# Performance work log

Measured on AMD Instinct MI355X. Metric: run time of the kernel, lower is better.

## Reference

```python
import jax, jax.numpy as jnp
import numpy as np
from functools import partial

B, L, H, OUT, T, NLAYERS = 1024, 128, 256, 64, 256, 2


def setup_inputs() -> dict:
    key = jax.random.key(0)
    ks = jax.random.split(key, 16)
    s = 0.05
    inp = {
        "latent": jax.random.normal(ks[0], (B, L), jnp.float32),
        # latent -> initial hidden / cell (Linear(L, H*num_layers))
        "w_lh": jax.random.normal(ks[1], (H * NLAYERS, L), jnp.float32) * s,
        "b_lh": jax.random.normal(ks[2], (H * NLAYERS,), jnp.float32) * s,
        "w_lc": jax.random.normal(ks[3], (H * NLAYERS, L), jnp.float32) * s,
        "b_lc": jax.random.normal(ks[4], (H * NLAYERS,), jnp.float32) * s,
        # LSTM layer 0 (input_size = L), PyTorch gate order i,f,g,o
        "w_ih0": jax.random.normal(ks[5], (4 * H, L), jnp.float32) * s,
        "w_hh0": jax.random.normal(ks[6], (4 * H, H), jnp.float32) * s,
        "b_ih0": jax.random.normal(ks[7], (4 * H,), jnp.float32) * s,
        "b_hh0": jax.random.normal(ks[8], (4 * H,), jnp.float32) * s,
        # LSTM layer 1 (input_size = H)
        "w_ih1": jax.random.normal(ks[9], (4 * H, H), jnp.float32) * s,
        "w_hh1": jax.random.normal(ks[10], (4 * H, H), jnp.float32) * s,
        "b_ih1": jax.random.normal(ks[11], (4 * H,), jnp.float32) * s,
        "b_hh1": jax.random.normal(ks[12], (4 * H,), jnp.float32) * s,
        # output projection Linear(H, OUT)
        "w_out": jax.random.normal(ks[13], (OUT, H), jnp.float32) * s,
        "b_out": jax.random.normal(ks[14], (OUT,), jnp.float32) * s,
    }
    return inp


def _lstm_layer(gx, h0, c0, w_hh):
    # gx: [T, B, 4H] precomputed input-projection + biases; scan the recurrence.
    def step(carry, gx_t):
        h, c = carry
        gates = gx_t + h @ w_hh.T  # [B, 4H]
        i, f, g, o = jnp.split(gates, 4, axis=-1)
        i, f, o = jax.nn.sigmoid(i), jax.nn.sigmoid(f), jax.nn.sigmoid(o)
        g = jnp.tanh(g)
        c = f * c + i * g
        h = o * jnp.tanh(c)
        return (h, c), h

    _, hs = jax.lax.scan(step, (h0, c0), gx)
    return hs  # [T, B, H]


def reference(latent, w_lh, b_lh, w_lc, b_lc,
              w_ih0, w_hh0, b_ih0, b_hh0,
              w_ih1, w_hh1, b_ih1, b_hh1,
              w_out, b_out):
    bsz = latent.shape[0]
    # initial states: [B, NLAYERS, H] -> per-layer [B, H]
    h = (latent @ w_lh.T + b_lh).reshape(bsz, NLAYERS, H)
    c = (latent @ w_lc.T + b_lc).reshape(bsz, NLAYERS, H)

    # decoder input is latent repeated T times; layer-0 input projection is
    # identical at every step, so compute it once and broadcast over time.
    gx0 = latent @ w_ih0.T + b_ih0 + b_hh0           # [B, 4H]
    gx0 = jnp.broadcast_to(gx0, (T, bsz, 4 * H))      # [T, B, 4H]
    hs0 = _lstm_layer(gx0, h[:, 0], c[:, 0], w_hh0)   # [T, B, H]

    # layer 1: time-varying input projection (dropout between layers is
    # inference-mode identity)
    gx1 = jnp.einsum('tbh,gh->tbg', hs0, w_ih1) + b_ih1 + b_hh1
    hs1 = _lstm_layer(gx1, h[:, 1], c[:, 1], w_hh1)   # [T, B, H]

    out = jnp.einsum('tbh,oh->tbo', hs1, w_out) + b_out  # [T, B, OUT]
    return jnp.transpose(out, (1, 0, 2))                 # [B, T, OUT]
```

## Files before the change

kernel.cpp:

```cpp
#include <hip/hip_runtime.h>


typedef float f32x4 __attribute__((ext_vector_type(4)));
typedef short bf16x8 __attribute__((ext_vector_type(8)));
typedef unsigned short u16;
typedef unsigned int u32;
typedef unsigned int u32x2 __attribute__((ext_vector_type(2)));
typedef unsigned int u32x4 __attribute__((ext_vector_type(4)));

#define OFF_LH   0
#define OFF_LC   65536
#define OFF_IH0  131072
#define OFF_HH0  262144
#define OFF_IH1  524288
#define OFF_HH1  786432
#define OFF_OUT  1048576

#define COMM_B   2228224
#define OBOX(bid,kind,slot) (COMM_B + ((((bid)*2+(kind))*2+(slot)) << 11))
#define FLAG_B   (COMM_B + 2097152)
#define FLAGQ(bid,kind) (FLAG_B + (((bid)*2+(kind)) << 4))
#define SPIN_LIMIT (1<<15)
#define HST 264

__device__ __forceinline__ u16 f2bf(float x){
  unsigned u = __builtin_bit_cast(unsigned, x);
  return (u16)((u + 0x7fffu + ((u >> 16) & 1u)) >> 16);
}

__global__ __launch_bounds__(256) void convert_swizzle(
    const float* __restrict__ src, u16* __restrict__ dst,
    int ntiles, int kbshift)
{
  int idx = blockIdx.x * 256 + threadIdx.x;
  int kblocks = 1 << kbshift;
  int n = ntiles << (kbshift + 9);
  if (idx >= n) return;
  int j    = idx & 7;
  int lane = (idx >> 3) & 63;
  int t3   = idx >> 9;
  int kt   = t3 & (kblocks - 1);
  int nt   = t3 >> kbshift;
  int row  = nt * 16 + (lane & 15);
  int k    = kt * 32 + (lane >> 4) * 8 + j;
  dst[idx] = f2bf(src[row * (kblocks * 32) + k]);
}

__device__ __forceinline__ f32x4 mfma16(bf16x8 a, bf16x8 b, f32x4 c){
  return __builtin_amdgcn_mfma_f32_16x16x32_bf16(a, b, c, 0, 0, 0);
}
__device__ __forceinline__ bf16x8 ld8(const u16* p){ return *(const bf16x8*)p; }
__device__ __forceinline__ float sigm(float x){ return 1.f/(1.f + __expf(-x)); }
__device__ __forceinline__ float tanh_f(float x){ return 1.f - 2.f/(__expf(2.f*x) + 1.f); }

#define ISSUE4(Q, seg, kt) \
  asm volatile( \
    "global_load_dwordx4 %0, %4, %8\n\t" \
    "global_load_dwordx4 %1, %5, %8\n\t" \
    "global_load_dwordx4 %2, %6, %8\n\t" \
    "global_load_dwordx4 %3, %7, %8" \
    : "=&v"(Q[0]), "=&v"(Q[1]), "=&v"(Q[2]), "=&v"(Q[3]) \
    : "v"(voffW +           (u32)((kt)*1024)), \
      "v"(voffW + 131072u + (u32)((kt)*1024)), \
      "v"(voffW + 262144u + (u32)((kt)*1024)), \
      "v"(voffW + 393216u + (u32)((kt)*1024)), \
      "s"(seg) \
    : "memory")

#define WAITN(Q, lit) \
  asm volatile("s_waitcnt vmcnt(" lit ")" \
    : "+v"(Q[0]), "+v"(Q[1]), "+v"(Q[2]), "+v"(Q[3]) :: "memory")
#define WAITC(Q) WAITN(Q, "12")

#define MFMA4(afrag, Q) { \
  acc0 = mfma16(afrag, Q[0], acc0); \
  acc1 = mfma16(afrag, Q[1], acc1); \
  acc2 = mfma16(afrag, Q[2], acc2); \
  acc3 = mfma16(afrag, Q[3], acc3); }

#define BARX() asm volatile("s_waitcnt lgkmcnt(0)\n\ts_barrier" ::: "memory")
#define VDRAIN() asm volatile("s_waitcnt vmcnt(0)" ::: "memory")

__device__ __forceinline__ void stflag(u32* p, u32 v){
  __hip_atomic_store(p, v, __ATOMIC_RELAXED, __HIP_MEMORY_SCOPE_AGENT);
}
__device__ __forceinline__ void pub8(char* p, u32 lo, u32 hi){
  u32x2 v = {lo, hi};
  asm volatile("global_store_dwordx2 %0, %1, off sc0 sc1" :: "v"(p), "v"(v) : "memory");
}

__device__ __forceinline__ void gatherF1(u16* hdst,
    const char* pay, const char* fq, int ps, int lane, u32 tgt, int* dead)
{
  if (!*dead){
    int gc = 0;
    for(;;){
      u32x4 fa;
      asm volatile(
        "global_load_dwordx4 %0, %1, off sc0 sc1\n\ts_waitcnt vmcnt(0)"
        : "=&v"(fa) : "v"(fq) : "memory");
      if (fa[0] >= tgt && fa[1] >= tgt && fa[2] >= tgt && fa[3] >= tgt) break;
      if (++gc > SPIN_LIMIT){ *dead = 1; break; }
    }
  }
  u32x4 q0, q1;
  asm volatile(
    "global_load_dwordx4 %0, %2, off sc0 sc1\n\t"
    "global_load_dwordx4 %1, %3, off sc0 sc1"
    : "=&v"(q0), "=&v"(q1)
    : "v"(pay), "v"(pay+16)
    : "memory");
  asm volatile("s_waitcnt vmcnt(0)" : "+v"(q0), "+v"(q1) :: "memory");
  const int r  = lane >> 4;
  const int cb = ps*64 + r*16;
  #pragma unroll
  for (int j = 0; j < 4; ++j){
    u32 lo = (j < 2) ? q0[2*j]   : q1[2*(j-2)];
    u32 hi = (j < 2) ? q0[2*j+1] : q1[2*(j-2)+1];
    int pl = (lane & 15)*4 + j;
    u16* dst = &hdst[((pl >> 4)*4)*HST + cb + (pl & 15)];
    dst[0]     = (u16)lo;
    dst[HST]   = (u16)(lo >> 16);
    dst[2*HST] = (u16)hi;
    dst[3*HST] = (u16)(hi >> 16);
  }
}

__global__ __launch_bounds__(512)
void lstm_fused(
    const float* __restrict__ latent,
    const float* __restrict__ b_lh, const float* __restrict__ b_lc,
    const float* __restrict__ b_ih0, const float* __restrict__ b_hh0,
    const float* __restrict__ b_ih1, const float* __restrict__ b_hh1,
    const float* __restrict__ b_out,
    const u16* __restrict__ ws,
    u16* __restrict__ comm,
    float* __restrict__ out)
{
  __shared__ __attribute__((aligned(16))) u16 h0f[2][16*HST];
  __shared__ __attribute__((aligned(16))) u16 h1f[3][16*HST];
  __shared__ __attribute__((aligned(16))) u16 lat_s[16*136];

  const u16* __restrict__ w_lh  = ws + OFF_LH;
  const u16* __restrict__ w_lc  = ws + OFF_LC;
  const u16* __restrict__ w_ih0 = ws + OFF_IH0;
  const u16* __restrict__ w_hh0 = ws + OFF_HH0;
  const u16* __restrict__ w_ih1 = ws + OFF_IH1;
  const u16* __restrict__ w_hh1 = ws + OFF_HH1;
  const u16* __restrict__ w_out = ws + OFF_OUT;

  const int tid  = threadIdx.x;
  const int w    = tid >> 6;
  const int lane = tid & 63;
  const int col  = lane & 15;
  const int quad = lane >> 4;
  const int bid  = blockIdx.x;
  const int s    = bid & 3;
  const int g    = bid >> 2;
  const int hct4 = w & 3;
  const int hrow = quad * 4;
  const int l8   = lane * 8;
  const int ctb  = s*64 + hct4*16;
  const u32 voffW = (u32)((s*4 + hct4) * 8192 + lane * 16);
  const int hreadR = col * HST + quad * 8;
  char* cm = (char*)comm;

  for (int i = tid; i < 16*128; i += 512){
    int b = i >> 7, k = i & 127;
    lat_s[b*136 + k] = f2bf(latent[(g*16 + b)*128 + k]);
  }
  __syncthreads();

  #pragma unroll 1
  for (int i = 0; i < 4; ++i){
    int task = w*4 + i;
    int layer = task >> 4, ct = task & 15;
    int nt = layer*16 + ct;
    float bias = b_lh[nt*16 + col];
    f32x4 a = {bias, bias, bias, bias};
    #pragma unroll
    for (int kt = 0; kt < 4; ++kt){
      bf16x8 la = ld8(&lat_s[col*136 + kt*32 + quad*8]);
      a = mfma16(la, ld8(w_lh + ((nt*4 + kt) << 9) + l8), a);
    }
    u16* dst = layer ? h1f[2] : h0f[1];
    #pragma unroll
    for (int rr = 0; rr < 4; ++rr)
      dst[(hrow + rr)*HST + ct*16 + col] = f2bf(a[rr]);
  }

  bf16x8 latA[4];
  #pragma unroll
  for (int kt = 0; kt < 4; ++kt)
    latA[kt] = ld8(&lat_s[col*136 + kt*32 + quad*8]);

  f32x4 gx0[4] = {};
  float bias1[4] = {};
  float c0[4] = {}, c1[4] = {};
  const float bo = (w == 0) ? b_out[s*16 + col] : 0.f;

  if (w < 4){
    { float bias = b_lc[ctb + col]; f32x4 a = {bias,bias,bias,bias};
      int nt0 = s*4 + hct4;
      #pragma unroll
      for (int kt = 0; kt < 4; ++kt)
        a = mfma16(latA[kt], ld8(w_lc + ((nt0*4 + kt) << 9) + l8), a);
      #pragma unroll
      for (int rr = 0; rr < 4; ++rr) c0[rr] = a[rr]; }
    #pragma unroll
    for (int g_ = 0; g_ < 4; ++g_){
      int nt = g_*16 + s*4 + hct4;
      float bias = b_ih0[nt*16 + col] + b_hh0[nt*16 + col];
      f32x4 a = {bias, bias, bias, bias};
      #pragma unroll
      for (int kt = 0; kt < 4; ++kt)
        a = mfma16(latA[kt], ld8(w_ih0 + ((nt*4 + kt) << 9) + l8), a);
      gx0[g_] = a;
    }
  } else {
    { float bias = b_lc[256 + ctb + col]; f32x4 a = {bias,bias,bias,bias};
      int nt1 = 16 + s*4 + hct4;
      #pragma unroll
      for (int kt = 0; kt < 4; ++kt)
        a = mfma16(latA[kt], ld8(w_lc + ((nt1*4 + kt) << 9) + l8), a);
      #pragma unroll
      for (int rr = 0; rr < 4; ++rr) c1[rr] = a[rr]; }
    #pragma unroll
    for (int g_ = 0; g_ < 4; ++g_){
      int nt = g_*16 + s*4 + hct4;
      bias1[g_] = b_ih1[nt*16 + col] + b_hh1[nt*16 + col];
    }
  }

  const int wl = w & 3;
  const int havep = (wl < 3);
  int ps = (wl < s) ? wl : wl + 1;
  if (!havep) ps = 0;
  const int kindm = (w < 4) ? 0 : 1;
  const char* ppay = cm + OBOX(g*4 + ps, kindm, 0) + lane*32;
  const char* fq   = cm + FLAGQ(g*4 + ps, kindm);
  u32* fmyw = (u32*)(cm + FLAGQ(bid, kindm)) + wl;
  char* pub_own = cm + OBOX(bid, kindm, 0) + hct4*512 + lane*8;
  int dead = 0;

  __syncthreads();

  bf16x8 Pq0[4], Pq1[4], Pq2[4], Pq3[4];
  f32x4 acc0, acc1, acc2, acc3;
  bf16x8 a0;
  if (w < 4){
    ISSUE4(Pq0, w_hh0, 0); ISSUE4(Pq1, w_hh0, 1);
    ISSUE4(Pq2, w_hh0, 2); ISSUE4(Pq3, w_hh0, 3);
    const u16* h0m1 = h0f[1];
    acc0 = gx0[0]; acc1 = gx0[1]; acc2 = gx0[2]; acc3 = gx0[3];
    WAITC(Pq0);      a0 = ld8(&h0m1[hreadR + 0*32]); MFMA4(a0, Pq0); ISSUE4(Pq0, w_hh0, 4);
    WAITC(Pq1);      a0 = ld8(&h0m1[hreadR + 1*32]); MFMA4(a0, Pq1); ISSUE4(Pq1, w_hh0, 5);
    WAITC(Pq2);      a0 = ld8(&h0m1[hreadR + 2*32]); MFMA4(a0, Pq2); ISSUE4(Pq2, w_hh0, 6);
    WAITC(Pq3);      a0 = ld8(&h0m1[hreadR + 3*32]); MFMA4(a0, Pq3); ISSUE4(Pq3, w_hh0, 7);
    WAITC(Pq0);      a0 = ld8(&h0m1[hreadR + 4*32]); MFMA4(a0, Pq0);
    WAITN(Pq1, "8"); a0 = ld8(&h0m1[hreadR + 5*32]); MFMA4(a0, Pq1);
    WAITN(Pq2, "4"); a0 = ld8(&h0m1[hreadR + 6*32]); MFMA4(a0, Pq2);
    WAITN(Pq3, "0"); a0 = ld8(&h0m1[hreadR + 7*32]); MFMA4(a0, Pq3);
    u32 plo = 0, phi = 0;
    #pragma unroll
    for (int rr = 0; rr < 4; ++rr){
      float ii = sigm(acc0[rr]);
      float ff = sigm(acc1[rr]);
      float gg = tanh_f(acc2[rr]);
      float oo = sigm(acc3[rr]);
      float c = ff*c0[rr] + ii*gg;
      c0[rr] = c;
      u16 hb = f2bf(oo * tanh_f(c));
      h0f[0][(hrow + rr)*HST + ctb + col] = hb;
      if (rr & 2) phi |= (u32)hb << ((rr & 1)*16);
      else        plo |= (u32)hb << ((rr & 1)*16);
    }
    pub8(pub_own, plo, phi);
    VDRAIN();
    __builtin_amdgcn_sched_barrier(0);
    if (lane == 0) stflag(fmyw, 1u);
    ISSUE4(Pq0, w_hh0, 0); ISSUE4(Pq1, w_hh0, 1);
    ISSUE4(Pq2, w_hh0, 2); ISSUE4(Pq3, w_hh0, 3);
  } else {
    ISSUE4(Pq0, w_hh1, 0); ISSUE4(Pq1, w_hh1, 1);
    ISSUE4(Pq2, w_hh1, 2); ISSUE4(Pq3, w_hh1, 3);
  }

  int m0 = 0, m1 = 2, m2 = 1;

  for (int t = 0; t < 256; ++t){
    const int p = t & 1;
    u16* h0c  = h0f[p];
    u16* h0n  = h0f[p ^ 1];
    u16* h1c  = h1f[m0];
    u16* h1pr = h1f[m1];

    if (w < 4){
      if (havep)
        gatherF1(h0c, ppay + (p << 11), fq, ps, lane, (u32)(t+1), &dead);
    } else if (t > 0 && havep){
      gatherF1(h1pr, ppay + ((p^1) << 11), fq, ps, lane, (u32)t, &dead);
    }
    BARX();

    if (w < 4){
      acc0 = gx0[0]; acc1 = gx0[1]; acc2 = gx0[2]; acc3 = gx0[3];
      WAITC(Pq0);      a0 = ld8(&h0c[hreadR + 0*32]); MFMA4(a0, Pq0); ISSUE4(Pq0, w_hh0, 4);
      WAITC(Pq1);      a0 = ld8(&h0c[hreadR + 1*32]); MFMA4(a0, Pq1); ISSUE4(Pq1, w_hh0, 5);
      WAITC(Pq2);      a0 = ld8(&h0c[hreadR + 2*32]); MFMA4(a0, Pq2); ISSUE4(Pq2, w_hh0, 6);
      WAITC(Pq3);      a0 = ld8(&h0c[hreadR + 3*32]); MFMA4(a0, Pq3); ISSUE4(Pq3, w_hh0, 7);
      WAITC(Pq0);      a0 = ld8(&h0c[hreadR + 4*32]); MFMA4(a0, Pq0);
      WAITN(Pq1, "8"); a0 = ld8(&h0c[hreadR + 5*32]); MFMA4(a0, Pq1);
      WAITN(Pq2, "4"); a0 = ld8(&h0c[hreadR + 6*32]); MFMA4(a0, Pq2);
      WAITN(Pq3, "0"); a0 = ld8(&h0c[hreadR + 7*32]); MFMA4(a0, Pq3);
      u32 plo = 0, phi = 0;
      #pragma unroll
      for (int rr = 0; rr < 4; ++rr){
        float ii = sigm(acc0[rr]);
        float ff = sigm(acc1[rr]);
        float gg = tanh_f(acc2[rr]);
        float oo = sigm(acc3[rr]);
        float c = ff*c0[rr] + ii*gg;
        c0[rr] = c;
        u16 hb = f2bf(oo * tanh_f(c));
        h0n[(hrow + rr)*HST + ctb + col] = hb;
        if (rr & 2) phi |= (u32)hb << ((rr & 1)*16);
        else        plo |= (u32)hb << ((rr & 1)*16);
      }
      pub8(pub_own + ((p^1) << 11), plo, phi);
      VDRAIN();
      __builtin_amdgcn_sched_barrier(0);
      if (lane == 0) stflag(fmyw, (u32)(t+2));
      ISSUE4(Pq0, w_hh0, 0); ISSUE4(Pq1, w_hh0, 1);
      ISSUE4(Pq2, w_hh0, 2); ISSUE4(Pq3, w_hh0, 3);
      if (w == 0 && t >= 2){
        const u16* h1o = h1f[m2];
        f32x4 o = {bo, bo, bo, bo};
        #pragma unroll
        for (int kt = 0; kt < 8; ++kt){
          bf16x8 af = ld8(&h1o[hreadR + kt*32]);
          o = mfma16(af, ld8(w_out + ((s*8 + kt) << 9) + l8), o);
        }
        #pragma unroll
        for (int rr = 0; rr < 4; ++rr){
          int b = g*16 + hrow + rr;
          __builtin_nontemporal_store(o[rr], &out[(b*256 + (t-2))*64 + s*16 + col]);
        }
      }
    } else {
      acc0 = (f32x4){bias1[0],bias1[0],bias1[0],bias1[0]};
      acc1 = (f32x4){bias1[1],bias1[1],bias1[1],bias1[1]};
      acc2 = (f32x4){bias1[2],bias1[2],bias1[2],bias1[2]};
      acc3 = (f32x4){bias1[3],bias1[3],bias1[3],bias1[3]};
      WAITC(Pq0);      a0 = ld8(&h1pr[hreadR + 0*32]); MFMA4(a0, Pq0); ISSUE4(Pq0, w_hh1, 4);
      WAITC(Pq1);      a0 = ld8(&h1pr[hreadR + 1*32]); MFMA4(a0, Pq1); ISSUE4(Pq1, w_hh1, 5);
      WAITC(Pq2);      a0 = ld8(&h1pr[hreadR + 2*32]); MFMA4(a0, Pq2); ISSUE4(Pq2, w_hh1, 6);
      WAITC(Pq3);      a0 = ld8(&h1pr[hreadR + 3*32]); MFMA4(a0, Pq3); ISSUE4(Pq3, w_hh1, 7);
      WAITC(Pq0);      a0 = ld8(&h1pr[hreadR + 4*32]); MFMA4(a0, Pq0); ISSUE4(Pq0, w_ih1, 0);
      WAITC(Pq1);      a0 = ld8(&h1pr[hreadR + 5*32]); MFMA4(a0, Pq1); ISSUE4(Pq1, w_ih1, 1);
      WAITC(Pq2);      a0 = ld8(&h1pr[hreadR + 6*32]); MFMA4(a0, Pq2); ISSUE4(Pq2, w_ih1, 2);
      WAITC(Pq3);      a0 = ld8(&h1pr[hreadR + 7*32]); MFMA4(a0, Pq3); ISSUE4(Pq3, w_ih1, 3);
      WAITC(Pq0);      a0 = ld8(&h0c[hreadR + 0*32]); MFMA4(a0, Pq0); ISSUE4(Pq0, w_ih1, 4);
      WAITC(Pq1);      a0 = ld8(&h0c[hreadR + 1*32]); MFMA4(a0, Pq1); ISSUE4(Pq1, w_ih1, 5);
      WAITC(Pq2);      a0 = ld8(&h0c[hreadR + 2*32]); MFMA4(a0, Pq2); ISSUE4(Pq2, w_ih1, 6);
      WAITC(Pq3);      a0 = ld8(&h0c[hreadR + 3*32]); MFMA4(a0, Pq3); ISSUE4(Pq3, w_ih1, 7);
      WAITC(Pq0);      a0 = ld8(&h0c[hreadR + 4*32]); MFMA4(a0, Pq0);
      WAITN(Pq1, "8"); a0 = ld8(&h0c[hreadR + 5*32]); MFMA4(a0, Pq1);
      WAITN(Pq2, "4"); a0 = ld8(&h0c[hreadR + 6*32]); MFMA4(a0, Pq2);
      WAITN(Pq3, "0"); a0 = ld8(&h0c[hreadR + 7*32]); MFMA4(a0, Pq3);
      u32 plo = 0, phi = 0;
      #pragma unroll
      for (int rr = 0; rr < 4; ++rr){
        float ii = sigm(acc0[rr]);
        float ff = sigm(acc1[rr]);
        float gg = tanh_f(acc2[rr]);
        float oo = sigm(acc3[rr]);
        float c = ff*c1[rr] + ii*gg;
        c1[rr] = c;
        u16 hb = f2bf(oo * tanh_f(c));
        h1c[(hrow + rr)*HST + ctb + col] = hb;
        if (rr & 2) phi |= (u32)hb << ((rr & 1)*16);
        else        plo |= (u32)hb << ((rr & 1)*16);
      }
      pub8(pub_own + (p << 11), plo, phi);
      VDRAIN();
      __builtin_amdgcn_sched_barrier(0);
      if (lane == 0) stflag(fmyw, (u32)(t+1));
      ISSUE4(Pq0, w_hh1, 0); ISSUE4(Pq1, w_hh1, 1);
      ISSUE4(Pq2, w_hh1, 2); ISSUE4(Pq3, w_hh1, 3);
    }
    BARX();

    int tm = m2; m2 = m1; m1 = m0; m0 = tm;
  }

  if (w >= 4){
    if (havep)
      gatherF1(h1f[0], ppay + (1 << 11), fq, ps, lane, 256u, &dead);
  } else if (w == 0){
    const u16* h1o = h1f[2];
    f32x4 o = {bo, bo, bo, bo};
    #pragma unroll
    for (int kt = 0; kt < 8; ++kt){
      bf16x8 af = ld8(&h1o[hreadR + kt*32]);
      o = mfma16(af, ld8(w_out + ((s*8 + kt) << 9) + l8), o);
    }
    #pragma unroll
    for (int rr = 0; rr < 4; ++rr){
      int b = g*16 + hrow + rr;
      __builtin_nontemporal_store(o[rr], &out[(b*256 + 254)*64 + s*16 + col]);
    }
  }
  BARX();
  if (w == 0){
    const u16* h1fin = h1f[0];
    f32x4 o = {bo, bo, bo, bo};
    #pragma unroll
    for (int kt = 0; kt < 8; ++kt){
      bf16x8 af = ld8(&h1fin[hreadR + kt*32]);
      o = mfma16(af, ld8(w_out + ((s*8 + kt) << 9) + l8), o);
    }
    #pragma unroll
    for (int rr = 0; rr < 4; ++rr){
      int b = g*16 + hrow + rr;
      __builtin_nontemporal_store(o[rr], &out[(b*256 + 255)*64 + s*16 + col]);
    }
  }
}

extern "C" void kernel_launch(void* const* d_in, const int* in_sizes, int n_in,
                              void* d_out, int out_size, void* d_ws, size_t ws_size,
                              hipStream_t stream)
{
  (void)in_sizes; (void)n_in; (void)out_size; (void)ws_size;
  const float* latent = (const float*)d_in[0];
  const float* w_lh   = (const float*)d_in[1];
  const float* b_lh   = (const float*)d_in[2];
  const float* w_lc   = (const float*)d_in[3];
  const float* b_lc   = (const float*)d_in[4];
  const float* w_ih0  = (const float*)d_in[5];
  const float* w_hh0  = (const float*)d_in[6];
  const float* b_ih0  = (const float*)d_in[7];
  const float* b_hh0  = (const float*)d_in[8];
  const float* w_ih1  = (const float*)d_in[9];
  const float* w_hh1  = (const float*)d_in[10];
  const float* b_ih1  = (const float*)d_in[11];
  const float* b_hh1  = (const float*)d_in[12];
  const float* w_out  = (const float*)d_in[13];
  const float* b_out  = (const float*)d_in[14];
  u16* ws = (u16*)d_ws;
  float* out = (float*)d_out;

  auto cvt = [&](const float* src, int off, int ntiles, int kbshift){
    int n = ntiles << (kbshift + 9);
    convert_swizzle<<<dim3((n + 255)/256), dim3(256), 0, stream>>>(src, ws + off, ntiles, kbshift);
  };
  cvt(w_lh,  OFF_LH,  32, 2);
  cvt(w_lc,  OFF_LC,  32, 2);
  cvt(w_ih0, OFF_IH0, 64, 2);
  cvt(w_hh0, OFF_HH0, 64, 3);
  cvt(w_ih1, OFF_IH1, 64, 3);
  cvt(w_hh1, OFF_HH1, 64, 3);
  cvt(w_out, OFF_OUT, 4, 3);

  hipMemsetAsync((char*)d_ws + FLAG_B, 0, 256*2*16, stream);

  lstm_fused<<<dim3(256), dim3(512), 0, stream>>>(latent, b_lh, b_lc, b_ih0, b_hh0,
                                                  b_ih1, b_hh1, b_out, ws, ws, out);
}
```

Before: 1.454 ms.

## Prefetch peer flags early and overlap payload loads with weight prefetch

Each wave now issues the flag load for its peer's handoff right after publishing its own step, so the next spin check often finds the flag already satisfied without a round trip. The per-step recurrent-weight prefetch (ISSUE4) is moved from the end of each step to after the payload loads are issued, and waits with vmcnt(16) so the payload can be consumed while the weight loads are still in flight. This aims to cut inter-block synchronisation latency on the serial recurrence. The trade-off is that weight prefetch now starts later, and correctness relies on vmcnt ordering assumptions in inline asm.

```diff
diff --git a/kernel.cpp b/kernel.cpp
--- a/kernel.cpp
+++ b/kernel.cpp
@@ -89,6 +89,22 @@
   asm volatile("global_store_dwordx2 %0, %1, off sc0 sc1" :: "v"(p), "v"(v) : "memory");
 }
 
+__device__ __forceinline__ void scat8(u16* hdst, u32x4 q0, u32x4 q1, int ps, int lane){
+  const int r  = lane >> 4;
+  const int cb = ps*64 + r*16;
+  #pragma unroll
+  for (int j = 0; j < 4; ++j){
+    u32 lo = (j < 2) ? q0[2*j]   : q1[2*(j-2)];
+    u32 hi = (j < 2) ? q0[2*j+1] : q1[2*(j-2)+1];
+    int pl = (lane & 15)*4 + j;
+    u16* dst = &hdst[((pl >> 4)*4)*HST + cb + (pl & 15)];
+    dst[0]     = (u16)lo;
+    dst[HST]   = (u16)(lo >> 16);
+    dst[2*HST] = (u16)hi;
+    dst[3*HST] = (u16)(hi >> 16);
+  }
+}
+
 __device__ __forceinline__ void gatherF1(u16* hdst,
     const char* pay, const char* fq, int ps, int lane, u32 tgt, int* dead)
 {
@@ -111,19 +127,7 @@
     : "v"(pay), "v"(pay+16)
     : "memory");
   asm volatile("s_waitcnt vmcnt(0)" : "+v"(q0), "+v"(q1) :: "memory");
-  const int r  = lane >> 4;
-  const int cb = ps*64 + r*16;
-  #pragma unroll
-  for (int j = 0; j < 4; ++j){
-    u32 lo = (j < 2) ? q0[2*j]   : q1[2*(j-2)];
-    u32 hi = (j < 2) ? q0[2*j+1] : q1[2*(j-2)+1];
-    int pl = (lane & 15)*4 + j;
-    u16* dst = &hdst[((pl >> 4)*4)*HST + cb + (pl & 15)];
-    dst[0]     = (u16)lo;
-    dst[HST]   = (u16)(lo >> 16);
-    dst[2*HST] = (u16)hi;
-    dst[3*HST] = (u16)(hi >> 16);
-  }
+  scat8(hdst, q0, q1, ps, lane);
 }
 
 __global__ __launch_bounds__(512)
@@ -242,6 +246,7 @@
   u32* fmyw = (u32*)(cm + FLAGQ(bid, kindm)) + wl;
   char* pub_own = cm + OBOX(bid, kindm, 0) + hct4*512 + lane*8;
   int dead = 0;
+  u32x4 fpre = {0,0,0,0};
 
   __syncthreads();
 
@@ -279,11 +284,9 @@
     VDRAIN();
     __builtin_amdgcn_sched_barrier(0);
     if (lane == 0) stflag(fmyw, 1u);
-    ISSUE4(Pq0, w_hh0, 0); ISSUE4(Pq1, w_hh0, 1);
-    ISSUE4(Pq2, w_hh0, 2); ISSUE4(Pq3, w_hh0, 3);
-  } else {
-    ISSUE4(Pq0, w_hh1, 0); ISSUE4(Pq1, w_hh1, 1);
-    ISSUE4(Pq2, w_hh1, 2); ISSUE4(Pq3, w_hh1, 3);
+    if (havep)
+      asm volatile("global_load_dwordx4 %0, %1, off sc0 sc1"
+        : "=&v"(fpre) : "v"(fq) : "memory");
   }
 
   int m0 = 0, m1 = 2, m2 = 1;
@@ -296,10 +299,63 @@
     u16* h1pr = h1f[m1];
 
     if (w < 4){
-      if (havep)
-        gatherF1(h0c, ppay + (p << 11), fq, ps, lane, (u32)(t+1), &dead);
-    } else if (t > 0 && havep){
-      gatherF1(h1pr, ppay + ((p^1) << 11), fq, ps, lane, (u32)t, &dead);
+      if (havep){
+        asm volatile("s_waitcnt vmcnt(0)" : "+v"(fpre) :: "memory");
+        u32 tgt = (u32)(t+1);
+        if (!dead && !(fpre[0] >= tgt && fpre[1] >= tgt && fpre[2] >= tgt && fpre[3] >= tgt)){
+          int gc = 0;
+          for(;;){
+            u32x4 fa;
+            asm volatile(
+              "global_load_dwordx4 %0, %1, off sc0 sc1\n\ts_waitcnt vmcnt(0)"
+              : "=&v"(fa) : "v"(fq) : "memory");
+            if (fa[0] >= tgt && fa[1] >= tgt && fa[2] >= tgt && fa[3] >= tgt) break;
+            if (++gc > SPIN_LIMIT){ dead = 1; break; }
+          }
+        }
+        const char* pp = ppay + (p << 11);
+        u32x4 q0, q1;
+        asm volatile(
+          "global_load_dwordx4 %0, %2, off sc0 sc1\n\t"
+          "global_load_dwordx4 %1, %3, off sc0 sc1"
+          : "=&v"(q0), "=&v"(q1) : "v"(pp), "v"(pp+16) : "memory");
+        ISSUE4(Pq0, w_hh0, 0); ISSUE4(Pq1, w_hh0, 1);
+        ISSUE4(Pq2, w_hh0, 2); ISSUE4(Pq3, w_hh0, 3);
+        asm volatile("s_waitcnt vmcnt(16)" : "+v"(q0), "+v"(q1) :: "memory");
+        scat8(h0c, q0, q1, ps, lane);
+      } else {
+        ISSUE4(Pq0, w_hh0, 0); ISSUE4(Pq1, w_hh0, 1);
+        ISSUE4(Pq2, w_hh0, 2); ISSUE4(Pq3, w_hh0, 3);
+      }
+    } else {
+      if (t > 0 && havep){
+        asm volatile("s_waitcnt vmcnt(0)" : "+v"(fpre) :: "memory");
+        u32 tgt = (u32)t;
+        if (!dead && !(fpre[0] >= tgt && fpre[1] >= tgt && fpre[2] >= tgt && fpre[3] >= tgt)){
+          int gc = 0;
+          for(;;){
+            u32x4 fa;
+            asm volatile(
+              "global_load_dwordx4 %0, %1, off sc0 sc1\n\ts_waitcnt vmcnt(0)"
+              : "=&v"(fa) : "v"(fq) : "memory");
+            if (fa[0] >= tgt && fa[1] >= tgt && fa[2] >= tgt && fa[3] >= tgt) break;
+            if (++gc > SPIN_LIMIT){ dead = 1; break; }
+          }
+        }
+        const char* pp = ppay + ((p^1) << 11);
+        u32x4 q0, q1;
+        asm volatile(
+          "global_load_dwordx4 %0, %2, off sc0 sc1\n\t"
+          "global_load_dwordx4 %1, %3, off sc0 sc1"
+          : "=&v"(q0), "=&v"(q1) : "v"(pp), "v"(pp+16) : "memory");
+        ISSUE4(Pq0, w_hh1, 0); ISSUE4(Pq1, w_hh1, 1);
+        ISSUE4(Pq2, w_hh1, 2); ISSUE4(Pq3, w_hh1, 3);
+        asm volatile("s_waitcnt vmcnt(16)" : "+v"(q0), "+v"(q1) :: "memory");
+        scat8(h1pr, q0, q1, ps, lane);
+      } else {
+        ISSUE4(Pq0, w_hh1, 0); ISSUE4(Pq1, w_hh1, 1);
+        ISSUE4(Pq2, w_hh1, 2); ISSUE4(Pq3, w_hh1, 3);
+      }
     }
     BARX();
 
@@ -331,8 +387,9 @@
       VDRAIN();
       __builtin_amdgcn_sched_barrier(0);
       if (lane == 0) stflag(fmyw, (u32)(t+2));
-      ISSUE4(Pq0, w_hh0, 0); ISSUE4(Pq1, w_hh0, 1);
-      ISSUE4(Pq2, w_hh0, 2); ISSUE4(Pq3, w_hh0, 3);
+      if (havep)
+        asm volatile("global_load_dwordx4 %0, %1, off sc0 sc1"
+          : "=&v"(fpre) : "v"(fq) : "memory");
       if (w == 0 && t >= 2){
         const u16* h1o = h1f[m2];
         f32x4 o = {bo, bo, bo, bo};
@@ -386,8 +443,9 @@
       VDRAIN();
       __builtin_amdgcn_sched_barrier(0);
       if (lane == 0) stflag(fmyw, (u32)(t+1));
-      ISSUE4(Pq0, w_hh1, 0); ISSUE4(Pq1, w_hh1, 1);
-      ISSUE4(Pq2, w_hh1, 2); ISSUE4(Pq3, w_hh1, 3);
+      if (havep)
+        asm volatile("global_load_dwordx4 %0, %1, off sc0 sc1"
+          : "=&v"(fpre) : "v"(fq) : "memory");
     }
     BARX();
 
```

Result: slower. 1.875 ms (+28.9%).

## Keep recurrent weight slices resident in registers instead of streaming each step

Applied to the files above, without the earlier changes.

Each wave now loads its slice of the recurrent weight matrix (w_hh0 or w_hh1) into 32 bf16x8 registers once before the time loop. The per-step global streaming of those weights is removed, and only w_ih1 is still streamed, through a two-deep queue. The layer-1 flag gather is inlined so the w_ih1 loads are issued before the payload scatter, overlapping them with the neighbour exchange. The cost is much higher VGPR pressure (128 extra registers), which risks spills at 512 threads per block.

```diff
diff --git a/kernel.cpp b/kernel.cpp
--- a/kernel.cpp
+++ b/kernel.cpp
@@ -70,7 +70,6 @@
 #define WAITN(Q, lit) \
   asm volatile("s_waitcnt vmcnt(" lit ")" \
     : "+v"(Q[0]), "+v"(Q[1]), "+v"(Q[2]), "+v"(Q[3]) :: "memory")
-#define WAITC(Q) WAITN(Q, "12")
 
 #define MFMA4(afrag, Q) { \
   acc0 = mfma16(afrag, Q[0], acc0); \
@@ -78,6 +77,12 @@
   acc2 = mfma16(afrag, Q[2], acc2); \
   acc3 = mfma16(afrag, Q[3], acc3); }
 
+#define MFMA4W(afrag, kt) { \
+  acc0 = mfma16(afrag, Wst[0*8+(kt)], acc0); \
+  acc1 = mfma16(afrag, Wst[1*8+(kt)], acc1); \
+  acc2 = mfma16(afrag, Wst[2*8+(kt)], acc2); \
+  acc3 = mfma16(afrag, Wst[3*8+(kt)], acc3); }
+
 #define BARX() asm volatile("s_waitcnt lgkmcnt(0)\n\ts_barrier" ::: "memory")
 #define VDRAIN() asm volatile("s_waitcnt vmcnt(0)" ::: "memory")
 
@@ -87,6 +92,22 @@
 __device__ __forceinline__ void pub8(char* p, u32 lo, u32 hi){
   u32x2 v = {lo, hi};
   asm volatile("global_store_dwordx2 %0, %1, off sc0 sc1" :: "v"(p), "v"(v) : "memory");
+}
+
+__device__ __forceinline__ void scat8(u16* hdst, u32x4 q0, u32x4 q1, int ps, int lane){
+  const int r  = lane >> 4;
+  const int cb = ps*64 + r*16;
+  #pragma unroll
+  for (int j = 0; j < 4; ++j){
+    u32 lo = (j < 2) ? q0[2*j]   : q1[2*(j-2)];
+    u32 hi = (j < 2) ? q0[2*j+1] : q1[2*(j-2)+1];
+    int pl = (lane & 15)*4 + j;
+    u16* dst = &hdst[((pl >> 4)*4)*HST + cb + (pl & 15)];
+    dst[0]     = (u16)lo;
+    dst[HST]   = (u16)(lo >> 16);
+    dst[2*HST] = (u16)hi;
+    dst[3*HST] = (u16)(hi >> 16);
+  }
 }
 
 __device__ __forceinline__ void gatherF1(u16* hdst,
@@ -111,19 +132,7 @@
     : "v"(pay), "v"(pay+16)
     : "memory");
   asm volatile("s_waitcnt vmcnt(0)" : "+v"(q0), "+v"(q1) :: "memory");
-  const int r  = lane >> 4;
-  const int cb = ps*64 + r*16;
-  #pragma unroll
-  for (int j = 0; j < 4; ++j){
-    u32 lo = (j < 2) ? q0[2*j]   : q1[2*(j-2)];
-    u32 hi = (j < 2) ? q0[2*j+1] : q1[2*(j-2)+1];
-    int pl = (lane & 15)*4 + j;
-    u16* dst = &hdst[((pl >> 4)*4)*HST + cb + (pl & 15)];
-    dst[0]     = (u16)lo;
-    dst[HST]   = (u16)(lo >> 16);
-    dst[2*HST] = (u16)hi;
-    dst[3*HST] = (u16)(hi >> 16);
-  }
+  scat8(hdst, q0, q1, ps, lane);
 }
 
 __global__ __launch_bounds__(512)
@@ -171,6 +180,19 @@
   }
   __syncthreads();
 
+  bf16x8 Wst[32];
+  {
+    const u16* wsrc = (w < 4) ? w_hh0 : w_hh1;
+    #pragma unroll
+    for (int g_ = 0; g_ < 4; ++g_){
+      #pragma unroll
+      for (int kt = 0; kt < 8; ++kt){
+        int nt = g_*16 + s*4 + hct4;
+        Wst[g_*8 + kt] = ld8(wsrc + ((nt*8 + kt) << 9) + l8);
+      }
+    }
+  }
+
   #pragma unroll 1
   for (int i = 0; i < 4; ++i){
     int task = w*4 + i;
@@ -245,22 +267,17 @@
 
   __syncthreads();
 
-  bf16x8 Pq0[4], Pq1[4], Pq2[4], Pq3[4];
+  bf16x8 Pq0[4], Pq1[4];
   f32x4 acc0, acc1, acc2, acc3;
   bf16x8 a0;
   if (w < 4){
-    ISSUE4(Pq0, w_hh0, 0); ISSUE4(Pq1, w_hh0, 1);
-    ISSUE4(Pq2, w_hh0, 2); ISSUE4(Pq3, w_hh0, 3);
     const u16* h0m1 = h0f[1];
     acc0 = gx0[0]; acc1 = gx0[1]; acc2 = gx0[2]; acc3 = gx0[3];
-    WAITC(Pq0);      a0 = ld8(&h0m1[hreadR + 0*32]); MFMA4(a0, Pq0); ISSUE4(Pq0, w_hh0, 4);
-    WAITC(Pq1);      a0 = ld8(&h0m1[hreadR + 1*32]); MFMA4(a0, Pq1); ISSUE4(Pq1, w_hh0, 5);
-    WAITC(Pq2);      a0 = ld8(&h0m1[hreadR + 2*32]); MFMA4(a0, Pq2); ISSUE4(Pq2, w_hh0, 6);
-    WAITC(Pq3);      a0 = ld8(&h0m1[hreadR + 3*32]); MFMA4(a0, Pq3); ISSUE4(Pq3, w_hh0, 7);
-    WAITC(Pq0);      a0 = ld8(&h0m1[hreadR + 4*32]); MFMA4(a0, Pq0);
-    WAITN(Pq1, "8"); a0 = ld8(&h0m1[hreadR + 5*32]); MFMA4(a0, Pq1);
-    WAITN(Pq2, "4"); a0 = ld8(&h0m1[hreadR + 6*32]); MFMA4(a0, Pq2);
-    WAITN(Pq3, "0"); a0 = ld8(&h0m1[hreadR + 7*32]); MFMA4(a0, Pq3);
+    #pragma unroll
+    for (int kt = 0; kt < 8; ++kt){
+      a0 = ld8(&h0m1[hreadR + kt*32]);
+      MFMA4W(a0, kt);
+    }
     u32 plo = 0, phi = 0;
     #pragma unroll
     for (int rr = 0; rr < 4; ++rr){
@@ -279,11 +296,6 @@
     VDRAIN();
     __builtin_amdgcn_sched_barrier(0);
     if (lane == 0) stflag(fmyw, 1u);
-    ISSUE4(Pq0, w_hh0, 0); ISSUE4(Pq1, w_hh0, 1);
-    ISSUE4(Pq2, w_hh0, 2); ISSUE4(Pq3, w_hh0, 3);
-  } else {
-    ISSUE4(Pq0, w_hh1, 0); ISSUE4(Pq1, w_hh1, 1);
-    ISSUE4(Pq2, w_hh1, 2); ISSUE4(Pq3, w_hh1, 3);
   }
 
   int m0 = 0, m1 = 2, m2 = 1;
@@ -298,21 +310,42 @@
     if (w < 4){
       if (havep)
         gatherF1(h0c, ppay + (p << 11), fq, ps, lane, (u32)(t+1), &dead);
-    } else if (t > 0 && havep){
-      gatherF1(h1pr, ppay + ((p^1) << 11), fq, ps, lane, (u32)t, &dead);
+    } else {
+      if (t > 0 && havep){
+        if (!dead){
+          int gc = 0;
+          u32 tgt = (u32)t;
+          for(;;){
+            u32x4 fa;
+            asm volatile(
+              "global_load_dwordx4 %0, %1, off sc0 sc1\n\ts_waitcnt vmcnt(0)"
+              : "=&v"(fa) : "v"(fq) : "memory");
+            if (fa[0] >= tgt && fa[1] >= tgt && fa[2] >= tgt && fa[3] >= tgt) break;
+            if (++gc > SPIN_LIMIT){ dead = 1; break; }
+          }
+        }
+        const char* pp = ppay + ((p^1) << 11);
+        u32x4 q0, q1;
+        asm volatile(
+          "global_load_dwordx4 %0, %2, off sc0 sc1\n\t"
+          "global_load_dwordx4 %1, %3, off sc0 sc1"
+          : "=&v"(q0), "=&v"(q1) : "v"(pp), "v"(pp+16) : "memory");
+        ISSUE4(Pq0, w_ih1, 0); ISSUE4(Pq1, w_ih1, 1);
+        asm volatile("s_waitcnt vmcnt(8)" : "+v"(q0), "+v"(q1) :: "memory");
+        scat8(h1pr, q0, q1, ps, lane);
+      } else {
+        ISSUE4(Pq0, w_ih1, 0); ISSUE4(Pq1, w_ih1, 1);
+      }
     }
     BARX();
 
     if (w < 4){
       acc0 = gx0[0]; acc1 = gx0[1]; acc2 = gx0[2]; acc3 = gx0[3];
-      WAITC(Pq0);      a0 = ld8(&h0c[hreadR + 0*32]); MFMA4(a0, Pq0); ISSUE4(Pq0, w_hh0, 4);
-      WAITC(Pq1);      a0 = ld8(&h0c[hreadR + 1*32]); MFMA4(a0, Pq1); ISSUE4(Pq1, w_hh0, 5);
-      WAITC(Pq2);      a0 = ld8(&h0c[hreadR + 2*32]); MFMA4(a0, Pq2); ISSUE4(Pq2, w_hh0, 6);
-      WAITC(Pq3);      a0 = ld8(&h0c[hreadR + 3*32]); MFMA4(a0, Pq3); ISSUE4(Pq3, w_hh0, 7);
-      WAITC(Pq0);      a0 = ld8(&h0c[hreadR + 4*32]); MFMA4(a0, Pq0);
-      WAITN(Pq1, "8"); a0 = ld8(&h0c[hreadR + 5*32]); MFMA4(a0, Pq1);
-      WAITN(Pq2, "4"); a0 = ld8(&h0c[hreadR + 6*32]); MFMA4(a0, Pq2);
-      WAITN(Pq3, "0"); a0 = ld8(&h0c[hreadR + 7*32]); MFMA4(a0, Pq3);
+      #pragma unroll
+      for (int kt = 0; kt < 8; ++kt){
+        a0 = ld8(&h0c[hreadR + kt*32]);
+        MFMA4W(a0, kt);
+      }
       u32 plo = 0, phi = 0;
       #pragma unroll
       for (int rr = 0; rr < 4; ++rr){
@@ -331,8 +364,6 @@
       VDRAIN();
       __builtin_amdgcn_sched_barrier(0);
       if (lane == 0) stflag(fmyw, (u32)(t+2));
-      ISSUE4(Pq0, w_hh0, 0); ISSUE4(Pq1, w_hh0, 1);
-      ISSUE4(Pq2, w_hh0, 2); ISSUE4(Pq3, w_hh0, 3);
       if (w == 0 && t >= 2){
         const u16* h1o = h1f[m2];
         f32x4 o = {bo, bo, bo, bo};
@@ -352,22 +383,19 @@
       acc1 = (f32x4){bias1[1],bias1[1],bias1[1],bias1[1]};
       acc2 = (f32x4){bias1[2],bias1[2],bias1[2],bias1[2]};
       acc3 = (f32x4){bias1[3],bias1[3],bias1[3],bias1[3]};
-      WAITC(Pq0);      a0 = ld8(&h1pr[hreadR + 0*32]); MFMA4(a0, Pq0); ISSUE4(Pq0, w_hh1, 4);
-      WAITC(Pq1);      a0 = ld8(&h1pr[hreadR + 1*32]); MFMA4(a0, Pq1); ISSUE4(Pq1, w_hh1, 5);
-      WAITC(Pq2);      a0 = ld8(&h1pr[hreadR + 2*32]); MFMA4(a0, Pq2); ISSUE4(Pq2, w_hh1, 6);
-      WAITC(Pq3);      a0 = ld8(&h1pr[hreadR + 3*32]); MFMA4(a0, Pq3); ISSUE4(Pq3, w_hh1, 7);
-      WAITC(Pq0);      a0 = ld8(&h1pr[hreadR + 4*32]); MFMA4(a0, Pq0); ISSUE4(Pq0, w_ih1, 0);
-      WAITC(Pq1);      a0 = ld8(&h1pr[hreadR + 5*32]); MFMA4(a0, Pq1); ISSUE4(Pq1, w_ih1, 1);
-      WAITC(Pq2);      a0 = ld8(&h1pr[hreadR + 6*32]); MFMA4(a0, Pq2); ISSUE4(Pq2, w_ih1, 2);
-      WAITC(Pq3);      a0 = ld8(&h1pr[hreadR + 7*32]); MFMA4(a0, Pq3); ISSUE4(Pq3, w_ih1, 3);
-      WAITC(Pq0);      a0 = ld8(&h0c[hreadR + 0*32]); MFMA4(a0, Pq0); ISSUE4(Pq0, w_ih1, 4);
-      WAITC(Pq1);      a0 = ld8(&h0c[hreadR + 1*32]); MFMA4(a0, Pq1); ISSUE4(Pq1, w_ih1, 5);
-      WAITC(Pq2);      a0 = ld8(&h0c[hreadR + 2*32]); MFMA4(a0, Pq2); ISSUE4(Pq2, w_ih1, 6);
-      WAITC(Pq3);      a0 = ld8(&h0c[hreadR + 3*32]); MFMA4(a0, Pq3); ISSUE4(Pq3, w_ih1, 7);
-      WAITC(Pq0);      a0 = ld8(&h0c[hreadR + 4*32]); MFMA4(a0, Pq0);
-      WAITN(Pq1, "8"); a0 = ld8(&h0c[hreadR + 5*32]); MFMA4(a0, Pq1);
-      WAITN(Pq2, "4"); a0 = ld8(&h0c[hreadR + 6*32]); MFMA4(a0, Pq2);
-      WAITN(Pq3, "0"); a0 = ld8(&h0c[hreadR + 7*32]); MFMA4(a0, Pq3);
+      #pragma unroll
+      for (int kt = 0; kt < 8; ++kt){
+        a0 = ld8(&h1pr[hreadR + kt*32]);
+        MFMA4W(a0, kt);
+      }
+      WAITN(Pq0,"4"); a0 = ld8(&h0c[hreadR + 0*32]); MFMA4(a0, Pq0); ISSUE4(Pq0, w_ih1, 2);
+      WAITN(Pq1,"4"); a0 = ld8(&h0c[hreadR + 1*32]); MFMA4(a0, Pq1); ISSUE4(Pq1, w_ih1, 3);
+      WAITN(Pq0,"4"); a0 = ld8(&h0c[hreadR + 2*32]); MFMA4(a0, Pq0); ISSUE4(Pq0, w_ih1, 4);
+      WAITN(Pq1,"4"); a0 = ld8(&h0c[hreadR + 3*32]); MFMA4(a0, Pq1); ISSUE4(Pq1, w_ih1, 5);
+      WAITN(Pq0,"4"); a0 = ld8(&h0c[hreadR + 4*32]); MFMA4(a0, Pq0); ISSUE4(Pq0, w_ih1, 6);
+      WAITN(Pq1,"4"); a0 = ld8(&h0c[hreadR + 5*32]); MFMA4(a0, Pq1); ISSUE4(Pq1, w_ih1, 7);
+      WAITN(Pq0,"4"); a0 = ld8(&h0c[hreadR + 6*32]); MFMA4(a0, Pq0);
+      WAITN(Pq1,"0"); a0 = ld8(&h0c[hreadR + 7*32]); MFMA4(a0, Pq1);
       u32 plo = 0, phi = 0;
       #pragma unroll
       for (int rr = 0; rr < 4; ++rr){
@@ -386,8 +414,6 @@
       VDRAIN();
       __builtin_amdgcn_sched_barrier(0);
       if (lane == 0) stflag(fmyw, (u32)(t+1));
-      ISSUE4(Pq0, w_hh1, 0); ISSUE4(Pq1, w_hh1, 1);
-      ISSUE4(Pq2, w_hh1, 2); ISSUE4(Pq3, w_hh1, 3);
     }
     BARX();
 
```

Result: faster. 1.332 ms (-8.4%).
